# Performance work log

Measured on AMD Instinct MI355X. Metric: run time of the kernel, lower is better.

## Reference

```python
import jax, jax.numpy as jnp
import numpy as np

B, S, D, H = 1, 2048, 4096, 32
HD = D // H
THETA = 10000.0
IN_SCALE = 0.1   # input_scale buffer
Q_SCALE = 0.1    # q_proj_scale buffer
K_SCALE = 0.1    # k_proj_scale buffer
V_SCALE = 0.1    # v_proj_scale buffer
OUT_SCALE = 0.1  # out_input_scale buffer


def _fake_q(x, scale, lo, hi):
    # round-to-int + clamp, kept in float (faithful to int8 fake-quant)
    return jnp.clip(jnp.round(x / scale), lo, hi)


def _w4a8_linear(x, qw, w_scale, in_scale):
    # int8 fake-quantized activation x int4-valued weight, dequant output
    qx = _fake_q(x, in_scale, -128, 127)
    return jnp.einsum('bsd,od->bso', qx, qw) * (in_scale * w_scale)


def _rope_tables(position_ids):
    inv_freq = 1.0 / (THETA ** (jnp.arange(0, HD, 2, dtype=jnp.float32) / HD))
    ang = position_ids.astype(jnp.float32)[..., None] * inv_freq  # [B,S,HD/2]
    emb = jnp.concatenate([ang, ang], axis=-1)                     # [B,S,HD]
    return jnp.cos(emb)[:, None], jnp.sin(emb)[:, None]            # [B,1,S,HD]


def _rotate_half(x):
    return jnp.concatenate([-x[..., HD // 2:], x[..., :HD // 2]], axis=-1)


def setup_inputs() -> dict:
    key = jax.random.key(0)
    ks = jax.random.split(key, 9)
    hidden_states = jax.random.normal(ks[0], (B, S, D), jnp.float32)
    def int4_w(k):
        return jnp.round(jax.random.uniform(k, (D, D), jnp.float32, -8.0, 7.0))
    def ch_scale(k):
        return jax.random.uniform(k, (D,), jnp.float32, 0.01, 0.03)
    wq, wk, wv, wo = int4_w(ks[1]), int4_w(ks[2]), int4_w(ks[3]), int4_w(ks[4])
    sq_w, sk_w, sv_w, so_w = ch_scale(ks[5]), ch_scale(ks[6]), ch_scale(ks[7]), ch_scale(ks[8])
    position_ids = jnp.arange(S, dtype=jnp.int32)[None, :]
    causal = jnp.tril(jnp.ones((S, S), dtype=bool))
    attention_mask = jnp.where(causal, 0.0, -1e9).astype(jnp.float32)[None, None]
    return dict(hidden_states=hidden_states, wq=wq, wk=wk, wv=wv, wo=wo,
                sq_w=sq_w, sk_w=sk_w, sv_w=sv_w, so_w=so_w,
                attention_mask=attention_mask, position_ids=position_ids)


def reference(hidden_states, wq, wk, wv, wo, sq_w, sk_w, sv_w, so_w,
              attention_mask, position_ids):
    # W4A8 dequant projections
    q = _w4a8_linear(hidden_states, wq, sq_w, IN_SCALE)
    k = _w4a8_linear(hidden_states, wk, sk_w, IN_SCALE)
    v = _w4a8_linear(hidden_states, wv, sv_w, IN_SCALE)
    q = q.reshape(B, S, H, HD).transpose(0, 2, 1, 3)  # [B,H,S,HD]
    k = k.reshape(B, S, H, HD).transpose(0, 2, 1, 3)
    v = v.reshape(B, S, H, HD).transpose(0, 2, 1, 3)
    # RoPE
    cos, sin = _rope_tables(position_ids)
    q = q * cos + _rotate_half(q) * sin
    k = k * cos + _rotate_half(k) * sin
    # int8 fake-quant of q/k/v, then dequant before matmuls
    q = _fake_q(q, Q_SCALE, -128, 127)
    k = _fake_q(k, K_SCALE, -128, 127)
    v = _fake_q(v, V_SCALE, -128, 127)
    scores = jnp.einsum('bhqd,bhkd->bhqk', q * Q_SCALE, k * K_SCALE) / np.sqrt(HD)
    scores = scores + attention_mask
    attn = jax.nn.softmax(scores.astype(jnp.float32), axis=-1)
    out = jnp.einsum('bhqk,bhkd->bhqd', attn, v * V_SCALE)
    out = out.transpose(0, 2, 1, 3).reshape(B, S, D)
    # o_proj input re-quantized to int8 with out_input_scale (clamp -127..127)
    out_q = _fake_q(out, OUT_SCALE, -127, 127)
    attn_output = jnp.einsum('bsd,od->bso', out_q, wo) * (OUT_SCALE * so_w)
    return attn_output
```

## Files before the change

kernel.cpp:

```cpp
#include <hip/hip_runtime.h>
#include <math.h>
#include <stdint.h>

#define S_LEN 2048
#define D_DIM 4096
#define NHEAD 32
#define HDIM  128

typedef int      v4i __attribute__((ext_vector_type(4)));
typedef float    v4f __attribute__((ext_vector_type(4)));
typedef _Float16 v8h __attribute__((ext_vector_type(8)));

__device__ __forceinline__ float quant128(float x) {
  return fminf(fmaxf(rintf(x / 0.1f), -128.f), 127.f);
}
__device__ __forceinline__ void gl_lds16(const void* g, void* l) {
  __builtin_amdgcn_global_load_lds(
      (const __attribute__((address_space(1))) void*)g,
      (__attribute__((address_space(3))) void*)l, 16, 0, 0);
}

__global__ __launch_bounds__(256) void quant_hidden_k(const float* __restrict__ in,
                                                      int8_t* __restrict__ out) {
  const int idx = blockIdx.x * 256 + threadIdx.x;
  const float4 v = ((const float4*)in)[idx];
  const int q0 = (int)quant128(v.x), q1 = (int)quant128(v.y);
  const int q2 = (int)quant128(v.z), q3 = (int)quant128(v.w);
  ((int*)out)[idx] = (q0 & 0xff) | ((q1 & 0xff) << 8) | ((q2 & 0xff) << 16) | ((q3 & 0xff) << 24);
}

__global__ __launch_bounds__(256) void wconv3_k(const float* __restrict__ a,
                                                const float* __restrict__ b,
                                                const float* __restrict__ c,
                                                int8_t* __restrict__ out) {
  const int which = blockIdx.x >> 14;
  const int sub = blockIdx.x & 16383;
  const float* src = (which == 0) ? a : (which == 1) ? b : c;
  const int idx = sub * 256 + threadIdx.x;
  const float4 v = ((const float4*)src)[idx];
  const int q0 = __float2int_rn(v.x), q1 = __float2int_rn(v.y);
  const int q2 = __float2int_rn(v.z), q3 = __float2int_rn(v.w);
  ((int*)out)[(size_t)which * 4194304 + idx] =
      (q0 & 0xff) | ((q1 & 0xff) << 8) | ((q2 & 0xff) << 16) | ((q3 & 0xff) << 24);
}

__global__ __launch_bounds__(256) void wconv_k(const float* __restrict__ in,
                                               int8_t* __restrict__ out) {
  const int idx = blockIdx.x * 256 + threadIdx.x;
  const float4 v = ((const float4*)in)[idx];
  const int q0 = __float2int_rn(v.x), q1 = __float2int_rn(v.y);
  const int q2 = __float2int_rn(v.z), q3 = __float2int_rn(v.w);
  ((int*)out)[idx] = (q0 & 0xff) | ((q1 & 0xff) << 8) | ((q2 & 0xff) << 16) | ((q3 & 0xff) << 24);
}

__global__ __launch_bounds__(256) void rope_tab_k(const int* __restrict__ pos,
                                                  float* __restrict__ ct,
                                                  float* __restrict__ st) {
  const int idx = blockIdx.x * 256 + threadIdx.x;
  const int s = idx >> 6, j = idx & 63;
  const float inv = exp2f((float)j * -0.20762050593046016f);
  const float a = (float)pos[s] * inv;
  float si, c;
  sincosf(a, &si, &c);
  ct[idx] = c;
  st[idx] = si;
}

template <int MODE>
__device__ __forceinline__ void gemm_body(
    int8_t* __restrict__ LS, const int8_t* __restrict__ A8,
    const int8_t* __restrict__ W8, const float* __restrict__ s0,
    const float* __restrict__ s1, const float* __restrict__ s2,
    const float* __restrict__ ctab, const float* __restrict__ stab,
    void* __restrict__ out0, void* __restrict__ out1, void* __restrict__ out2,
    int nwg) {
  int8_t* const Abase = LS;
  int8_t* const Bbase = LS + 49152;

  const int t = threadIdx.x;
  const int w = t >> 6, lane = t & 63, g = lane >> 4, l15 = lane & 15;
  const int wm = w >> 2, wn = w & 3;

  const int bid = blockIdx.x;
  const int lb = (bid & 7) * (nwg >> 3) + (bid >> 3);
  const int within = lb & 15, g16 = lb >> 4;
  const int bm = ((g16 & 3) * 4 + (within >> 2)) * 128;
  const int bn = ((g16 >> 2) * 4 + (within & 3)) * 256;

  const int rowo = lane >> 3;
  const int schunk = ((lane & 7) ^ rowo) * 16;
  const int8_t* srcA[2];
  const int8_t* srcB[4];
#pragma unroll
  for (int i = 0; i < 2; ++i)
    srcA[i] = A8 + (size_t)(bm + w * 16 + i * 8 + rowo) * D_DIM + schunk;
#pragma unroll
  for (int i = 0; i < 4; ++i)
    srcB[i] = W8 + (size_t)(bn + w * 32 + i * 8 + rowo) * D_DIM + schunk;

#define STAGE(KT, BI)                                                       \
  {                                                                         \
    const int kof_ = (KT) * 128;                                            \
    int8_t* Ad_ = Abase + (BI) * 16384 + w * 2048;                          \
    int8_t* Bd_ = Bbase + (BI) * 32768 + w * 4096;                          \
    _Pragma("unroll") for (int i_ = 0; i_ < 2; ++i_)                        \
        gl_lds16(srcA[i_] + kof_, Ad_ + i_ * 1024);                         \
    _Pragma("unroll") for (int i_ = 0; i_ < 4; ++i_)                        \
        gl_lds16(srcB[i_] + kof_, Bd_ + i_ * 1024);                         \
  }

  const int nc0 = (wn & 1) * 32 + (wn >> 1) * 128;

  const int coff0 = (g ^ (l15 & 7)) * 16;
  const int coff1 = ((4 | g) ^ (l15 & 7)) * 16;
  const int aoff = (wm * 64 + l15) * 128;
  int boff[4];
#pragma unroll
  for (int ni = 0; ni < 4; ++ni)
    boff[ni] = (nc0 + (ni & 1) * 16 + (ni >> 1) * 64 + l15) * 128;

  v4i fa[4], fb[4];
  v4i ga[4], gb[4];

#define RD(FA, FB, BI, COFF)                                                \
  {                                                                         \
    const int8_t* Ab_ = Abase + (BI) * 16384;                               \
    const int8_t* Bb_ = Bbase + (BI) * 32768;                               \
    _Pragma("unroll") for (int mi_ = 0; mi_ < 4; ++mi_)                     \
        FA[mi_] = *(const v4i*)(Ab_ + aoff + mi_ * 2048 + (COFF));          \
    _Pragma("unroll") for (int ni_ = 0; ni_ < 4; ++ni_)                     \
        FB[ni_] = *(const v4i*)(Bb_ + boff[ni_] + (COFF));                  \
  }

#define MM(FA, FB)                                                          \
  _Pragma("unroll") for (int mi_ = 0; mi_ < 4; ++mi_)                       \
  _Pragma("unroll") for (int ni_ = 0; ni_ < 4; ++ni_)                       \
      acc[mi_][ni_] = __builtin_amdgcn_mfma_i32_16x16x64_i8(                \
          FA[mi_], FB[ni_], acc[mi_][ni_], 0, 0, 0);

  v4i acc[4][4];
#pragma unroll
  for (int mi = 0; mi < 4; ++mi)
#pragma unroll
    for (int ni = 0; ni < 4; ++ni) acc[mi][ni] = (v4i){0, 0, 0, 0};

  STAGE(0, 0)
  STAGE(1, 1)
  asm volatile("s_waitcnt vmcnt(6)" ::: "memory");
  __builtin_amdgcn_s_barrier();
  __builtin_amdgcn_sched_barrier(0);
  RD(fa, fb, 0, coff0)

  for (int t3 = 0; t3 < 33; t3 += 3) {
#pragma unroll
    for (int u = 0; u < 3; ++u) {
      const int kt = t3 + u;
      if (kt < 32) {
        if (kt + 2 < 32) STAGE(kt + 2, ((u + 2) % 3))
        RD(ga, gb, u, coff1)
        __builtin_amdgcn_s_setprio(1);
        MM(fa, fb)
        MM(ga, gb)
        __builtin_amdgcn_s_setprio(0);
        if (kt + 2 < 32)
          asm volatile("s_waitcnt vmcnt(6)" ::: "memory");
        else
          asm volatile("s_waitcnt vmcnt(0)" ::: "memory");
        __builtin_amdgcn_s_barrier();
        __builtin_amdgcn_sched_barrier(0);
        if (kt + 1 < 32) RD(fa, fb, ((u + 1) % 3), coff0)
      }
    }
  }
#undef STAGE
#undef RD
#undef MM

  const int srow0 = bm + wm * 64;
  if (MODE == 1) {
    float* dst = (float*)out0;
#pragma unroll
    for (int ni = 0; ni < 4; ++ni) {
      const int col = bn + nc0 + (ni & 1) * 16 + (ni >> 1) * 64 + l15;
      const float sc = 0.1f * s0[col];
#pragma unroll
      for (int mi = 0; mi < 4; ++mi)
#pragma unroll
        for (int r = 0; r < 4; ++r)
          dst[(size_t)(srow0 + mi * 16 + g * 4 + r) * D_DIM + col] =
              (float)acc[mi][ni][r] * sc;
    }
  } else {
    const int seg = bn >> 12;
    const int bcol = bn & 4095;
    if (seg == 2) {
      _Float16* dst = (_Float16*)out2;
#pragma unroll
      for (int ni = 0; ni < 4; ++ni) {
        const int col = bcol + nc0 + (ni & 1) * 16 + (ni >> 1) * 64 + l15;
        const float scv = 0.1f * s2[col];
#pragma unroll
        for (int mi = 0; mi < 4; ++mi)
#pragma unroll
          for (int r = 0; r < 4; ++r) {
            const int s = srow0 + mi * 16 + g * 4 + r;
            dst[(size_t)col * S_LEN + s] = (_Float16)quant128((float)acc[mi][ni][r] * scv);
          }
      }
    } else {
      const float* wsc = seg ? s1 : s0;
      int8_t* dst = seg ? (int8_t*)out1 : (int8_t*)out0;
      const int hb = bcol + (wn >> 1) * 128;
#pragma unroll
      for (int ni = 0; ni < 2; ++ni) {
        const int dlo = (wn & 1) * 32 + ni * 16 + l15;
        const int clo = hb + dlo;
        const float sc0 = 0.1f * wsc[clo];
        const float sc1 = 0.1f * wsc[clo + 64];
#pragma unroll
        for (int mi = 0; mi < 4; ++mi)
#pragma unroll
          for (int r = 0; r < 4; ++r) {
            const int s = srow0 + mi * 16 + g * 4 + r;
            const float c = ctab[s * 64 + dlo];
            const float si = stab[s * 64 + dlo];
            const float x1 = (float)acc[mi][ni][r] * sc0;
            const float x2 = (float)acc[mi][ni + 2][r] * sc1;
            dst[(size_t)s * D_DIM + clo] = (int8_t)quant128(x1 * c - x2 * si);
            dst[(size_t)s * D_DIM + clo + 64] = (int8_t)quant128(x2 * c + x1 * si);
          }
      }
    }
  }
}

__global__ __launch_bounds__(512, 1) void gemm_qkv(
    const int8_t* __restrict__ A8, const int8_t* __restrict__ W8,
    const float* __restrict__ s0, const float* __restrict__ s1,
    const float* __restrict__ s2, const float* __restrict__ ctab,
    const float* __restrict__ stab, void* __restrict__ out0,
    void* __restrict__ out1, void* __restrict__ out2) {
  __shared__ __align__(16) int8_t LS[3 * 16384 + 3 * 32768];
  gemm_body<0>(LS, A8, W8, s0, s1, s2, ctab, stab, out0, out1, out2, 768);
}

__global__ __launch_bounds__(512, 1) void gemm_out(
    const int8_t* __restrict__ A8, const int8_t* __restrict__ W8,
    const float* __restrict__ s0, const float* __restrict__ ctab,
    const float* __restrict__ stab, void* __restrict__ out0) {
  __shared__ __align__(16) int8_t LS[3 * 16384 + 3 * 32768];
  gemm_body<1>(LS, A8, W8, s0, s0, s0, ctab, stab, out0, out0, out0, 256);
}

__global__ __launch_bounds__(256, 2) void attn_v7(
    const int8_t* __restrict__ q8, const int8_t* __restrict__ k8,
    const _Float16* __restrict__ vT, int8_t* __restrict__ o8) {
  __shared__ __align__(16) int8_t Kls[3][8192];
  __shared__ __align__(16) int8_t Vls[3][16384];
  const int j = 31 - blockIdx.x;
  const int h = blockIdx.y;
  const int t = threadIdx.x;
  const int w = t >> 6, lane = t & 63, g = lane >> 4, l15 = lane & 15;
  const int T = j + 1;
  const int q0 = (4 * j + w) * 16;
  const int q_lane = q0 + l15;
  const float SSCALE = 8.838834764831845e-4f;
  const v8h vones = {(_Float16)1, (_Float16)1, (_Float16)1, (_Float16)1,
                     (_Float16)1, (_Float16)1, (_Float16)1, (_Float16)1};

  int k_src[2], v_src[4], kv_dst[4];
#pragma unroll
  for (int i = 0; i < 2; ++i) {
    const int lin = i * 256 + t;
    const int s = lin >> 3;
    const int cs = (lin & 7) ^ (s & 7);
    const int key = ((s >> 5) & 1) * 32 + ((s >> 3) & 1) * 16 +
                    ((s >> 2) & 1) * 8 + ((s >> 4) & 1) * 4 + (s & 3);
    k_src[i] = key * D_DIM + cs * 16;
  }
#pragma unroll
  for (int i = 0; i < 4; ++i) {
    const int lin = i * 256 + t;
    const int d = lin >> 3;
    const int cs = (lin & 7) ^ (d & 7);
    v_src[i] = d * S_LEN + cs * 8;
    kv_dst[i] = lin * 16;
  }
  const int8_t* kbg = k8 + (size_t)h * HDIM;
  const _Float16* vbg = vT + (size_t)h * HDIM * S_LEN;

  auto stage = [&](int kt, int b) {
    const int8_t* ks = kbg + (size_t)kt * (64 * D_DIM);
    const _Float16* vs = vbg + kt * 64;
#pragma unroll
    for (int i = 0; i < 2; ++i) gl_lds16(ks + k_src[i], &Kls[b][kv_dst[i]]);
#pragma unroll
    for (int i = 0; i < 4; ++i) gl_lds16(vs + v_src[i], &Vls[b][kv_dst[i]]);
  };

  const v4i qa0 = *(const v4i*)(q8 + (size_t)q_lane * D_DIM + h * HDIM + g * 16);
  const v4i qa1 = *(const v4i*)(q8 + (size_t)q_lane * D_DIM + h * HDIM + 64 + g * 16);

  v4f o[8];
#pragma unroll
  for (int n = 0; n < 8; ++n) o[n] = (v4f){0.f, 0.f, 0.f, 0.f};
  v4f lacc = (v4f){0.f, 0.f, 0.f, 0.f};
  float m_i = -INFINITY;

  stage(0, 0);
  if (T > 1) stage(1, 1);

  int bi = 0;
  for (int kt = 0; kt < T; ++kt) {
    if (kt + 1 < T)
      asm volatile("s_waitcnt vmcnt(6)" ::: "memory");
    else
      asm volatile("s_waitcnt vmcnt(0)" ::: "memory");
    __builtin_amdgcn_s_barrier();
    __builtin_amdgcn_sched_barrier(0);
    if (kt + 2 < T) stage(kt + 2, bi >= 1 ? bi - 1 : bi + 2);

    const int ksw = (l15 & 7);
    float sc[4][4];
#pragma unroll
    for (int nt = 0; nt < 4; ++nt) {
      const int8_t* kr = &Kls[bi][(nt * 16 + l15) * 128];
      const v4i kb0 = *(const v4i*)(kr + ((g ^ ksw) * 16));
      const v4i kb1 = *(const v4i*)(kr + (((4 + g) ^ ksw) * 16));
      v4i c = (v4i){0, 0, 0, 0};
      c = __builtin_amdgcn_mfma_i32_16x16x64_i8(kb0, qa0, c, 0, 0, 0);
      c = __builtin_amdgcn_mfma_i32_16x16x64_i8(kb1, qa1, c, 0, 0, 0);
#pragma unroll
      for (int r = 0; r < 4; ++r) {
        float s = (float)c[r] * SSCALE;
        if (kt == T - 1) {
          const int key = kt * 64 + ((nt >> 1) << 5) + ((g >> 1) << 4) +
                          ((g & 1) << 3) + ((nt & 1) << 2) + r;
          if (key > q_lane) s = -1.0e30f;
        }
        sc[nt][r] = s;
      }
    }
    float mx = fmaxf(fmaxf(fmaxf(sc[0][0], sc[0][1]), fmaxf(sc[0][2], sc[0][3])),
                     fmaxf(fmaxf(sc[1][0], sc[1][1]), fmaxf(sc[1][2], sc[1][3])));
    mx = fmaxf(mx, fmaxf(fmaxf(fmaxf(sc[2][0], sc[2][1]), fmaxf(sc[2][2], sc[2][3])),
                         fmaxf(fmaxf(sc[3][0], sc[3][1]), fmaxf(sc[3][2], sc[3][3]))));
    mx = fmaxf(mx, __shfl_xor(mx, 16));
    mx = fmaxf(mx, __shfl_xor(mx, 32));
    const float mnew = fmaxf(m_i, mx);
    const float alpha = __expf(m_i - mnew);
    m_i = mnew;

    float p[4][4];
#pragma unroll
    for (int nt = 0; nt < 4; ++nt)
#pragma unroll
      for (int r = 0; r < 4; ++r) p[nt][r] = __expf(sc[nt][r] - m_i);

    v8h ph0, ph1;
#pragma unroll
    for (int e = 0; e < 8; ++e) {
      ph0[e] = (_Float16)p[e >> 2][e & 3];
      ph1[e] = (_Float16)p[2 + (e >> 2)][e & 3];
    }
    float a_r[4];
#pragma unroll
    for (int r = 0; r < 4; ++r)
      a_r[r] = __shfl(alpha, (lane & 48) | (g * 4 + r));
#pragma unroll
    for (int n = 0; n < 8; ++n)
#pragma unroll
      for (int r = 0; r < 4; ++r) o[n][r] *= a_r[r];
#pragma unroll
    for (int r = 0; r < 4; ++r) lacc[r] *= a_r[r];

    __builtin_amdgcn_s_setprio(1);
    lacc = __builtin_amdgcn_mfma_f32_16x16x32_f16(ph0, vones, lacc, 0, 0, 0);
    lacc = __builtin_amdgcn_mfma_f32_16x16x32_f16(ph1, vones, lacc, 0, 0, 0);
#pragma unroll
    for (int nt = 0; nt < 8; ++nt) {
      const int8_t* vr = &Vls[bi][(nt * 16 + l15) * 128];
      const v8h v0 = *(const v8h*)(vr + ((g ^ ksw) * 16));
      const v8h v1 = *(const v8h*)(vr + (((4 + g) ^ ksw) * 16));
      o[nt] = __builtin_amdgcn_mfma_f32_16x16x32_f16(ph0, v0, o[nt], 0, 0, 0);
      o[nt] = __builtin_amdgcn_mfma_f32_16x16x32_f16(ph1, v1, o[nt], 0, 0, 0);
    }
    __builtin_amdgcn_s_setprio(0);

    bi = (bi == 2) ? 0 : bi + 1;
  }

#pragma unroll
  for (int r = 0; r < 4; ++r) {
    const float rL = 1.0f / lacc[r];
    const size_t row = (size_t)(q0 + g * 4 + r) * D_DIM + h * HDIM;
#pragma unroll
    for (int nt = 0; nt < 8; ++nt) {
      const int q = (int)fminf(fmaxf(rintf(o[nt][r] * rL), -127.f), 127.f);
      o8[row + nt * 16 + l15] = (int8_t)q;
    }
  }
}

extern "C" void kernel_launch(void* const* d_in, const int* in_sizes, int n_in,
                              void* d_out, int out_size, void* d_ws, size_t ws_size,
                              hipStream_t stream) {
  (void)in_sizes; (void)n_in; (void)out_size; (void)ws_size;
  const float* hidden = (const float*)d_in[0];
  const float* wq = (const float*)d_in[1];
  const float* wk = (const float*)d_in[2];
  const float* wv = (const float*)d_in[3];
  const float* wo = (const float*)d_in[4];
  const float* sq = (const float*)d_in[5];
  const float* sk = (const float*)d_in[6];
  const float* sv = (const float*)d_in[7];
  const float* so = (const float*)d_in[8];
  const int* pos = (const int*)d_in[10];
  float* out = (float*)d_out;

  char* ws = (char*)d_ws;
  int8_t* h8 = (int8_t*)ws;
  int8_t* q8 = (int8_t*)(ws + (8ull << 20));
  int8_t* k8 = (int8_t*)(ws + (16ull << 20));
  _Float16* vT = (_Float16*)(ws + (24ull << 20));
  int8_t* w8a = (int8_t*)(ws + (40ull << 20));
  int8_t* w8b = (int8_t*)(ws + (56ull << 20));
  int8_t* w8c = (int8_t*)(ws + (72ull << 20));
  float* ctab = (float*)(ws + (88ull << 20));
  float* stab = (float*)(ws + (88ull << 20) + (512ull << 10));
  int8_t* o8 = h8;

  hipLaunchKernelGGL(rope_tab_k, dim3(512), dim3(256), 0, stream, pos, ctab, stab);
  hipLaunchKernelGGL(quant_hidden_k, dim3(8192), dim3(256), 0, stream, hidden, h8);
  hipLaunchKernelGGL(wconv3_k, dim3(49152), dim3(256), 0, stream, wq, wk, wv, w8a);

  hipLaunchKernelGGL(gemm_qkv, dim3(768), dim3(512), 0, stream, h8, w8a,
                     sq, sk, sv, ctab, stab, (void*)q8, (void*)k8, (void*)vT);
  hipLaunchKernelGGL(wconv_k, dim3(16384), dim3(256), 0, stream, wo, w8a);
  hipLaunchKernelGGL(attn_v7, dim3(32, 32), dim3(256), 0, stream, q8, k8, vT, o8);
  hipLaunchKernelGGL(gemm_out, dim3(256), dim3(512), 0, stream, o8, w8a,
                     so, ctab, stab, (void*)out);
}
```

Measured before the change: 522.9 us.

## Prepack activations in MFMA fragment layout and load A directly to registers

The quantized hidden states and the attention output are now written in a tiled layout that matches the int8 MFMA A-fragment order, so each lane loads its A operands straight from global memory into registers instead of staging them through LDS. Only the B (weight) tiles stay in LDS, now double-buffered, so LDS drops to 64KB and the launch bounds no longer force one block per CU. This trades LDS traffic and occupancy limits for more global loads issued per lane and extra barriers in the K loop.

```diff
diff --git a/kernel.cpp b/kernel.cpp
--- a/kernel.cpp
+++ b/kernel.cpp
@@ -26,7 +26,13 @@
   const float4 v = ((const float4*)in)[idx];
   const int q0 = (int)quant128(v.x), q1 = (int)quant128(v.y);
   const int q2 = (int)quant128(v.z), q3 = (int)quant128(v.w);
-  ((int*)out)[idx] = (q0 & 0xff) | ((q1 & 0xff) << 8) | ((q2 & 0xff) << 16) | ((q3 & 0xff) << 24);
+  const int pack =
+      (q0 & 0xff) | ((q1 & 0xff) << 8) | ((q2 & 0xff) << 16) | ((q3 & 0xff) << 24);
+  const int row = idx >> 10;
+  const int k4 = (idx & 1023) << 2;
+  const int dst = ((row >> 4) * 64 + (k4 >> 6)) * 1024 +
+                  (((k4 >> 4) & 3) * 16 + (row & 15)) * 16 + (k4 & 15);
+  *(int*)(out + dst) = pack;
 }
 
 __global__ __launch_bounds__(256) void wconv3_k(const float* __restrict__ a,
@@ -74,9 +80,6 @@
     const float* __restrict__ ctab, const float* __restrict__ stab,
     void* __restrict__ out0, void* __restrict__ out1, void* __restrict__ out2,
     int nwg) {
-  int8_t* const Abase = LS;
-  int8_t* const Bbase = LS + 49152;
-
   const int t = threadIdx.x;
   const int w = t >> 6, lane = t & 63, g = lane >> 4, l15 = lane & 15;
   const int wm = w >> 2, wn = w & 3;
@@ -89,92 +92,81 @@
 
   const int rowo = lane >> 3;
   const int schunk = ((lane & 7) ^ rowo) * 16;
-  const int8_t* srcA[2];
   const int8_t* srcB[4];
-#pragma unroll
-  for (int i = 0; i < 2; ++i)
-    srcA[i] = A8 + (size_t)(bm + w * 16 + i * 8 + rowo) * D_DIM + schunk;
 #pragma unroll
   for (int i = 0; i < 4; ++i)
     srcB[i] = W8 + (size_t)(bn + w * 32 + i * 8 + rowo) * D_DIM + schunk;
 
-#define STAGE(KT, BI)                                                       \
+#define STAGEB(KT, BI)                                                      \
   {                                                                         \
     const int kof_ = (KT) * 128;                                            \
-    int8_t* Ad_ = Abase + (BI) * 16384 + w * 2048;                          \
-    int8_t* Bd_ = Bbase + (BI) * 32768 + w * 4096;                          \
-    _Pragma("unroll") for (int i_ = 0; i_ < 2; ++i_)                        \
-        gl_lds16(srcA[i_] + kof_, Ad_ + i_ * 1024);                         \
+    int8_t* Bd_ = LS + (BI) * 32768 + w * 4096;                             \
     _Pragma("unroll") for (int i_ = 0; i_ < 4; ++i_)                        \
         gl_lds16(srcB[i_] + kof_, Bd_ + i_ * 1024);                         \
   }
 
   const int nc0 = (wn & 1) * 32 + (wn >> 1) * 128;
-
-  const int coff0 = (g ^ (l15 & 7)) * 16;
-  const int coff1 = ((4 | g) ^ (l15 & 7)) * 16;
-  const int aoff = (wm * 64 + l15) * 128;
   int boff[4];
 #pragma unroll
   for (int ni = 0; ni < 4; ++ni)
     boff[ni] = (nc0 + (ni & 1) * 16 + (ni >> 1) * 64 + l15) * 128;
 
-  v4i fa[4], fb[4];
-  v4i ga[4], gb[4];
-
-#define RD(FA, FB, BI, COFF)                                                \
+  const int amt0 = (bm >> 4) + wm * 4;
+
+#define AFLOAD(SET, KT)                                                     \
+  _Pragma("unroll") for (int mi_ = 0; mi_ < 4; ++mi_)                       \
+  _Pragma("unroll") for (int kk_ = 0; kk_ < 2; ++kk_)                       \
+      SET[mi_][kk_] = *(const v4i*)(A8 +                                    \
+          ((size_t)((amt0 + mi_) * 64 + (KT) * 2 + kk_) << 10) + lane * 16);
+
+  v4i acc[4][4];
+#pragma unroll
+  for (int mi = 0; mi < 4; ++mi)
+#pragma unroll
+    for (int ni = 0; ni < 4; ++ni) acc[mi][ni] = (v4i){0, 0, 0, 0};
+
+  v4i afA[4][2], afB[4][2];
+
+#define STEP(KT, BI, CUR, NXT)                                              \
   {                                                                         \
-    const int8_t* Ab_ = Abase + (BI) * 16384;                               \
-    const int8_t* Bb_ = Bbase + (BI) * 32768;                               \
-    _Pragma("unroll") for (int mi_ = 0; mi_ < 4; ++mi_)                     \
-        FA[mi_] = *(const v4i*)(Ab_ + aoff + mi_ * 2048 + (COFF));          \
-    _Pragma("unroll") for (int ni_ = 0; ni_ < 4; ++ni_)                     \
-        FB[ni_] = *(const v4i*)(Bb_ + boff[ni_] + (COFF));                  \
-  }
-
-#define MM(FA, FB)                                                          \
-  _Pragma("unroll") for (int mi_ = 0; mi_ < 4; ++mi_)                       \
-  _Pragma("unroll") for (int ni_ = 0; ni_ < 4; ++ni_)                       \
-      acc[mi_][ni_] = __builtin_amdgcn_mfma_i32_16x16x64_i8(                \
-          FA[mi_], FB[ni_], acc[mi_][ni_], 0, 0, 0);
-
-  v4i acc[4][4];
-#pragma unroll
-  for (int mi = 0; mi < 4; ++mi)
-#pragma unroll
-    for (int ni = 0; ni < 4; ++ni) acc[mi][ni] = (v4i){0, 0, 0, 0};
-
-  STAGE(0, 0)
-  STAGE(1, 1)
-  asm volatile("s_waitcnt vmcnt(6)" ::: "memory");
-  __builtin_amdgcn_s_barrier();
-  __builtin_amdgcn_sched_barrier(0);
-  RD(fa, fb, 0, coff0)
-
-  for (int t3 = 0; t3 < 33; t3 += 3) {
-#pragma unroll
-    for (int u = 0; u < 3; ++u) {
-      const int kt = t3 + u;
-      if (kt < 32) {
-        if (kt + 2 < 32) STAGE(kt + 2, ((u + 2) % 3))
-        RD(ga, gb, u, coff1)
-        __builtin_amdgcn_s_setprio(1);
-        MM(fa, fb)
-        MM(ga, gb)
-        __builtin_amdgcn_s_setprio(0);
-        if (kt + 2 < 32)
-          asm volatile("s_waitcnt vmcnt(6)" ::: "memory");
-        else
-          asm volatile("s_waitcnt vmcnt(0)" ::: "memory");
-        __builtin_amdgcn_s_barrier();
-        __builtin_amdgcn_sched_barrier(0);
-        if (kt + 1 < 32) RD(fa, fb, ((u + 1) % 3), coff0)
-      }
-    }
-  }
-#undef STAGE
-#undef RD
-#undef MM
+    if ((KT) < 31)                                                          \
+      asm volatile("s_waitcnt vmcnt(12)" ::: "memory");                     \
+    else                                                                    \
+      asm volatile("s_waitcnt vmcnt(8)" ::: "memory");                      \
+    __builtin_amdgcn_s_barrier();                                           \
+    __builtin_amdgcn_sched_barrier(0);                                      \
+    if ((KT) + 1 < 32) AFLOAD(NXT, (KT) + 1)                                \
+    _Pragma("unroll") for (int kk_ = 0; kk_ < 2; ++kk_) {                   \
+      v4i bf_[4];                                                           \
+      const int coff_ = (((kk_ << 2) | g) ^ (l15 & 7)) * 16;                \
+      const int8_t* Bb_ = LS + (BI) * 32768;                                \
+      _Pragma("unroll") for (int ni_ = 0; ni_ < 4; ++ni_)                   \
+          bf_[ni_] = *(const v4i*)(Bb_ + boff[ni_] + coff_);                \
+      __builtin_amdgcn_s_setprio(1);                                        \
+      _Pragma("unroll") for (int mi_ = 0; mi_ < 4; ++mi_)                   \
+      _Pragma("unroll") for (int ni_ = 0; ni_ < 4; ++ni_)                   \
+          acc[mi_][ni_] = __builtin_amdgcn_mfma_i32_16x16x64_i8(            \
+              CUR[mi_][kk_], bf_[ni_], acc[mi_][ni_], 0, 0, 0);             \
+      __builtin_amdgcn_s_setprio(0);                                        \
+    }                                                                       \
+    if ((KT) + 2 < 32) {                                                    \
+      __builtin_amdgcn_s_barrier();                                         \
+      __builtin_amdgcn_sched_barrier(0);                                    \
+      STAGEB((KT) + 2, BI)                                                  \
+    }                                                                       \
+  }
+
+  STAGEB(0, 0)
+  STAGEB(1, 1)
+  AFLOAD(afA, 0)
+
+  for (int kt = 0; kt < 32; kt += 2) {
+    STEP(kt, 0, afA, afB)
+    STEP(kt + 1, 1, afB, afA)
+  }
+#undef STEP
+#undef AFLOAD
+#undef STAGEB
 
   const int srow0 = bm + wm * 64;
   if (MODE == 1) {
@@ -234,21 +226,21 @@
   }
 }
 
-__global__ __launch_bounds__(512, 1) void gemm_qkv(
+__global__ __launch_bounds__(512) void gemm_qkv(
     const int8_t* __restrict__ A8, const int8_t* __restrict__ W8,
     const float* __restrict__ s0, const float* __restrict__ s1,
     const float* __restrict__ s2, const float* __restrict__ ctab,
     const float* __restrict__ stab, void* __restrict__ out0,
     void* __restrict__ out1, void* __restrict__ out2) {
-  __shared__ __align__(16) int8_t LS[3 * 16384 + 3 * 32768];
+  __shared__ __align__(16) int8_t LS[2 * 32768];
   gemm_body<0>(LS, A8, W8, s0, s1, s2, ctab, stab, out0, out1, out2, 768);
 }
 
-__global__ __launch_bounds__(512, 1) void gemm_out(
+__global__ __launch_bounds__(512) void gemm_out(
     const int8_t* __restrict__ A8, const int8_t* __restrict__ W8,
     const float* __restrict__ s0, const float* __restrict__ ctab,
     const float* __restrict__ stab, void* __restrict__ out0) {
-  __shared__ __align__(16) int8_t LS[3 * 16384 + 3 * 32768];
+  __shared__ __align__(16) int8_t LS[2 * 32768];
   gemm_body<1>(LS, A8, W8, s0, s0, s0, ctab, stab, out0, out0, out0, 256);
 }
 
@@ -393,11 +385,12 @@
 #pragma unroll
   for (int r = 0; r < 4; ++r) {
     const float rL = 1.0f / lacc[r];
-    const size_t row = (size_t)(q0 + g * 4 + r) * D_DIM + h * HDIM;
+    const int row = q0 + g * 4 + r;
+    const int base = ((row >> 4) * 64 + h * 2) * 1024 + (row & 15) * 16 + l15;
 #pragma unroll
     for (int nt = 0; nt < 8; ++nt) {
       const int q = (int)fminf(fmaxf(rintf(o[nt][r] * rL), -127.f), 127.f);
-      o8[row + nt * 16 + l15] = (int8_t)q;
+      o8[base + (nt >> 2) * 1024 + (nt & 3) * 256] = (int8_t)q;
     }
   }
 }
```

Result: slower. 569.6 us (+8.9%).

## Widen attention blocks to 8 waves sharing each K/V tile over 128 queries

Applied to the files above, without the earlier changes.

The attention kernel now launches 512-thread blocks covering 128 query rows (8 waves), so each staged K/V tile is reused by twice as many waves. Loads are split across more threads (one K load and two V loads per thread), and causal masking is applied on the last two key tiles. The GEMM kernels also drop their min-blocks launch bound hint. The tradeoff is coarser blocks, fewer blocks in the grid, and waves in a block that do unequal work on the diagonal.

```diff
diff --git a/kernel.cpp b/kernel.cpp
--- a/kernel.cpp
+++ b/kernel.cpp
@@ -234,7 +234,7 @@
   }
 }
 
-__global__ __launch_bounds__(512, 1) void gemm_qkv(
+__global__ __launch_bounds__(512) void gemm_qkv(
     const int8_t* __restrict__ A8, const int8_t* __restrict__ W8,
     const float* __restrict__ s0, const float* __restrict__ s1,
     const float* __restrict__ s2, const float* __restrict__ ctab,
@@ -244,7 +244,7 @@
   gemm_body<0>(LS, A8, W8, s0, s1, s2, ctab, stab, out0, out1, out2, 768);
 }
 
-__global__ __launch_bounds__(512, 1) void gemm_out(
+__global__ __launch_bounds__(512) void gemm_out(
     const int8_t* __restrict__ A8, const int8_t* __restrict__ W8,
     const float* __restrict__ s0, const float* __restrict__ ctab,
     const float* __restrict__ stab, void* __restrict__ out0) {
@@ -252,39 +252,37 @@
   gemm_body<1>(LS, A8, W8, s0, s0, s0, ctab, stab, out0, out0, out0, 256);
 }
 
-__global__ __launch_bounds__(256, 2) void attn_v7(
+__global__ __launch_bounds__(512, 4) void attn_v8(
     const int8_t* __restrict__ q8, const int8_t* __restrict__ k8,
     const _Float16* __restrict__ vT, int8_t* __restrict__ o8) {
   __shared__ __align__(16) int8_t Kls[3][8192];
   __shared__ __align__(16) int8_t Vls[3][16384];
-  const int j = 31 - blockIdx.x;
+  const int jj = 15 - blockIdx.x;
   const int h = blockIdx.y;
   const int t = threadIdx.x;
   const int w = t >> 6, lane = t & 63, g = lane >> 4, l15 = lane & 15;
-  const int T = j + 1;
-  const int q0 = (4 * j + w) * 16;
+  const int T = 2 * jj + 2;
+  const int q0 = (jj * 8 + w) * 16;
   const int q_lane = q0 + l15;
   const float SSCALE = 8.838834764831845e-4f;
   const v8h vones = {(_Float16)1, (_Float16)1, (_Float16)1, (_Float16)1,
                      (_Float16)1, (_Float16)1, (_Float16)1, (_Float16)1};
 
-  int k_src[2], v_src[4], kv_dst[4];
+  const int ks_slot = t >> 3;
+  const int ks_cs = (t & 7) ^ (ks_slot & 7);
+  const int ks_key = ((ks_slot >> 5) & 1) * 32 + ((ks_slot >> 3) & 1) * 16 +
+                     ((ks_slot >> 2) & 1) * 8 + ((ks_slot >> 4) & 1) * 4 +
+                     (ks_slot & 3);
+  const int k_src = ks_key * D_DIM + ks_cs * 16;
+  const int k_dst = t * 16;
+  int v_src[2], v_dst[2];
 #pragma unroll
   for (int i = 0; i < 2; ++i) {
-    const int lin = i * 256 + t;
-    const int s = lin >> 3;
-    const int cs = (lin & 7) ^ (s & 7);
-    const int key = ((s >> 5) & 1) * 32 + ((s >> 3) & 1) * 16 +
-                    ((s >> 2) & 1) * 8 + ((s >> 4) & 1) * 4 + (s & 3);
-    k_src[i] = key * D_DIM + cs * 16;
-  }
-#pragma unroll
-  for (int i = 0; i < 4; ++i) {
-    const int lin = i * 256 + t;
+    const int lin = i * 512 + t;
     const int d = lin >> 3;
     const int cs = (lin & 7) ^ (d & 7);
     v_src[i] = d * S_LEN + cs * 8;
-    kv_dst[i] = lin * 16;
+    v_dst[i] = lin * 16;
   }
   const int8_t* kbg = k8 + (size_t)h * HDIM;
   const _Float16* vbg = vT + (size_t)h * HDIM * S_LEN;
@@ -292,10 +290,9 @@
   auto stage = [&](int kt, int b) {
     const int8_t* ks = kbg + (size_t)kt * (64 * D_DIM);
     const _Float16* vs = vbg + kt * 64;
-#pragma unroll
-    for (int i = 0; i < 2; ++i) gl_lds16(ks + k_src[i], &Kls[b][kv_dst[i]]);
-#pragma unroll
-    for (int i = 0; i < 4; ++i) gl_lds16(vs + v_src[i], &Vls[b][kv_dst[i]]);
+    gl_lds16(ks + k_src, &Kls[b][k_dst]);
+#pragma unroll
+    for (int i = 0; i < 2; ++i) gl_lds16(vs + v_src[i], &Vls[b][v_dst[i]]);
   };
 
   const v4i qa0 = *(const v4i*)(q8 + (size_t)q_lane * D_DIM + h * HDIM + g * 16);
@@ -313,7 +310,7 @@
   int bi = 0;
   for (int kt = 0; kt < T; ++kt) {
     if (kt + 1 < T)
-      asm volatile("s_waitcnt vmcnt(6)" ::: "memory");
+      asm volatile("s_waitcnt vmcnt(3)" ::: "memory");
     else
       asm volatile("s_waitcnt vmcnt(0)" ::: "memory");
     __builtin_amdgcn_s_barrier();
@@ -333,7 +330,7 @@
 #pragma unroll
       for (int r = 0; r < 4; ++r) {
         float s = (float)c[r] * SSCALE;
-        if (kt == T - 1) {
+        if (kt >= T - 2) {
           const int key = kt * 64 + ((nt >> 1) << 5) + ((g >> 1) << 4) +
                           ((g & 1) << 3) + ((nt & 1) << 2) + r;
           if (key > q_lane) s = -1.0e30f;
@@ -437,7 +434,7 @@
   hipLaunchKernelGGL(gemm_qkv, dim3(768), dim3(512), 0, stream, h8, w8a,
                      sq, sk, sv, ctab, stab, (void*)q8, (void*)k8, (void*)vT);
   hipLaunchKernelGGL(wconv_k, dim3(16384), dim3(256), 0, stream, wo, w8a);
-  hipLaunchKernelGGL(attn_v7, dim3(32, 32), dim3(256), 0, stream, q8, k8, vT, o8);
+  hipLaunchKernelGGL(attn_v8, dim3(16, 32), dim3(512), 0, stream, q8, k8, vT, o8);
   hipLaunchKernelGGL(gemm_out, dim3(256), dim3(512), 0, stream, o8, w8a,
                      so, ctab, stab, (void*)out);
 }
```

After: 505.2 us. 3.4% less time.
